# Kernel tuning notes

Hardware: AMD Instinct MI355X
Metric: run time of the kernel (lower is better)

Reference implementation:

```python
import jax, jax.numpy as jnp
import numpy as np

B, N, D = 64, 8192, 128
REPLACE = 0.0  # stands in for torch.inf default; kept finite for numerics


def setup_inputs() -> dict:
    key = jax.random.key(0)
    k1, k2 = jax.random.split(key)
    X = jax.random.normal(k1, (B, N, D), dtype=jnp.float32)
    # mask True == position masked OUT (module computes ~mask to get valid)
    mask = jax.random.randint(k2, (B, N), 0, 2) == 1
    W = jnp.ones((D,), dtype=jnp.float32)
    b = jnp.zeros((D,), dtype=jnp.float32)
    return {"X": X, "mask": mask, "W": W, "b": b}


def reference(X, mask, W, b):
    # valid positions: ~mask, broadcast across feature dim
    valid = (~mask)[:, :, None].astype(X.dtype)          # [B, N, 1]
    count = jnp.sum(valid, axis=1)                       # [B, 1]
    mean = jnp.sum(X * valid, axis=1) / count            # [B, D]
    centered = X - mean[:, None, :]                      # [B, N, D]
    # torch masked std is unbiased (ddof=1)
    var = jnp.sum((centered * centered) * valid, axis=1) / (count - 1.0)
    std = jnp.sqrt(var)                                  # [B, D]
    normed = centered / std[:, None, :]                  # [B, N, D]
    # diag_embed(W) + F.linear == elementwise affine
    out = normed * W + b
    # masked positions were filled with REPLACE before the affine step
    out = jnp.where(mask[:, :, None], REPLACE * W + b, out)
    return out
```

## Files before the change

### kernel.cpp

```cpp
#include <hip/hip_runtime.h>

#define B_ 64
#define N_ 8192
#define D_ 128
#define D4 (D_ / 4)
#define NCHUNKS 16
#define CHUNK (N_ / NCHUNKS)

typedef float v4f __attribute__((ext_vector_type(4)));

#define WS_SUMP  0
#define WS_SQP   (B_ * NCHUNKS * D_)
#define WS_CNTP  (2 * B_ * NCHUNKS * D_)
#define WS_SCALE (2 * B_ * NCHUNKS * D_ + B_ * NCHUNKS)
#define WS_SHIFT (WS_SCALE + B_ * D_)

__global__ __launch_bounds__(256) void reduce_kernel(
        const float* __restrict__ X, const int* __restrict__ mask,
        float* __restrict__ ws) {
    const int b   = blockIdx.x;
    const int cy  = blockIdx.y;
    const int tid = threadIdx.x;
    const int q   = tid & 31;
    const int sub = tid >> 5;
    const int n0  = cy * CHUNK;

    const v4f* __restrict__ Xr = (const v4f*)(X + (size_t)b * N_ * D_);
    const int* __restrict__ mr = mask + b * N_;

    v4f s  = (v4f)(0.f);
    v4f ss = (v4f)(0.f);
    float cnt = 0.f;

    #pragma unroll 4
    for (int k = 0; k < CHUNK / 8; ++k) {
        const int n = n0 + sub + 8 * k;
        const float v = (mr[n] == 0) ? 1.0f : 0.0f;
        v4f x = Xr[(size_t)n * D4 + q];
        x *= v;
        s += x;
        ss += x * x;
        cnt += v;
    }

    __shared__ v4f sh_s[8][32];
    __shared__ v4f sh_ss[8][32];
    __shared__ float sh_c[8];
    sh_s[sub][q]  = s;
    sh_ss[sub][q] = ss;
    if (q == 0) sh_c[sub] = cnt;
    __syncthreads();

    if (sub == 0) {
        v4f ts = s, tss = ss;
        for (int k = 1; k < 8; ++k) {
            ts  += sh_s[k][q];
            tss += sh_ss[k][q];
        }
        v4f* __restrict__ sump = (v4f*)(ws + WS_SUMP);
        v4f* __restrict__ sqp  = (v4f*)(ws + WS_SQP);
        const int slot = (b * NCHUNKS + cy) * D4 + q;
        sump[slot] = ts;
        sqp[slot]  = tss;
    }
    if (tid == 0) {
        float c = 0.f;
        for (int k = 0; k < 8; ++k) c += sh_c[k];
        ws[WS_CNTP + b * NCHUNKS + cy] = c;
    }
}

__global__ __launch_bounds__(256) void finalize_kernel(
        const float* __restrict__ W, const float* __restrict__ bias,
        float* __restrict__ ws) {
    const float* __restrict__ sump = ws + WS_SUMP;
    const float* __restrict__ sqp  = ws + WS_SQP;
    const float* __restrict__ cntp = ws + WS_CNTP;
    float* __restrict__ scale = ws + WS_SCALE;
    float* __restrict__ shift = ws + WS_SHIFT;

    const int i = blockIdx.x * blockDim.x + threadIdx.x;
    if (i >= B_ * D_) return;
    const int b = i >> 7;
    const int d = i & (D_ - 1);

    float c = 0.f, s = 0.f, sq = 0.f;
    #pragma unroll
    for (int cy = 0; cy < NCHUNKS; ++cy) {
        c  += cntp[b * NCHUNKS + cy];
        s  += sump[(b * NCHUNKS + cy) * D_ + d];
        sq += sqp [(b * NCHUNKS + cy) * D_ + d];
    }
    const float mean = s / c;
    const float var  = (sq - s * mean) / (c - 1.0f);
    const float sc   = W[d] * rsqrtf(var);
    scale[i] = sc;
    shift[i] = bias[d] - mean * sc;
}

__global__ __launch_bounds__(256) void normalize_kernel(
        const float* __restrict__ X, const int* __restrict__ mask,
        const float* __restrict__ ws, const float* __restrict__ bias,
        float* __restrict__ out) {
    const v4f* __restrict__ X4 = (const v4f*)X;
    v4f* __restrict__ O4 = (v4f*)out;
    const v4f* __restrict__ S4 = (const v4f*)(ws + WS_SCALE);
    const v4f* __restrict__ H4 = (const v4f*)(ws + WS_SHIFT);
    const v4f* __restrict__ B4 = (const v4f*)bias;

    const long long total = (long long)B_ * N_ * D4;
    long long i = (long long)blockIdx.x * blockDim.x + threadIdx.x;
    const long long stride = (long long)gridDim.x * blockDim.x;

    for (; i < total; i += stride) {
        const int row = (int)(i >> 5);
        const int c   = (int)(i & 31);
        const int b   = row >> 13;
        const int m   = mask[row];
        const v4f x  = X4[i];
        const v4f sc = S4[b * D4 + c];
        const v4f sh = H4[b * D4 + c];
        const v4f bb = B4[c];
        const v4f norm = x * sc + sh;
        v4f o;
        o.x = m ? bb.x : norm.x;
        o.y = m ? bb.y : norm.y;
        o.z = m ? bb.z : norm.z;
        o.w = m ? bb.w : norm.w;
        __builtin_nontemporal_store(o, &O4[i]);
    }
}

extern "C" void kernel_launch(void* const* d_in, const int* in_sizes, int n_in,
                              void* d_out, int out_size, void* d_ws, size_t ws_size,
                              hipStream_t stream) {
    const float* X    = (const float*)d_in[0];
    const int*   mask = (const int*)d_in[1];
    const float* W    = (const float*)d_in[2];
    const float* bias = (const float*)d_in[3];
    float* out = (float*)d_out;
    float* ws  = (float*)d_ws;

    reduce_kernel<<<dim3(B_, NCHUNKS), 256, 0, stream>>>(X, mask, ws);

    finalize_kernel<<<(B_ * D_ + 255) / 256, 256, 0, stream>>>(W, bias, ws);

    normalize_kernel<<<4096, 256, 0, stream>>>(X, mask, ws, bias, out);
}
```

Baseline: 493.3 us.

## Skip loads of masked rows and flatten normalize grid

The reduction kernel now stages the chunk's mask into shared memory, fully unrolls the row loop, and only loads X for valid rows. Chunk count is doubled so more blocks are launched. The normalize kernel drops its grid-stride loop and uses one thread per vec4 with a branch, so masked rows skip reading X and the scale/shift. This aims to cut memory traffic for roughly half the rows, at the cost of divergent control flow and a larger launch grid.

```diff
diff --git a/kernel.cpp b/kernel.cpp
--- a/kernel.cpp
+++ b/kernel.cpp
@@ -4,7 +4,7 @@
 #define N_ 8192
 #define D_ 128
 #define D4 (D_ / 4)
-#define NCHUNKS 16
+#define NCHUNKS 32
 #define CHUNK (N_ / NCHUNKS)
 
 typedef float v4f __attribute__((ext_vector_type(4)));
@@ -25,22 +25,27 @@
     const int sub = tid >> 5;
     const int n0  = cy * CHUNK;
 
-    const v4f* __restrict__ Xr = (const v4f*)(X + (size_t)b * N_ * D_);
-    const int* __restrict__ mr = mask + b * N_;
+    __shared__ float valid[CHUNK];
+    valid[tid] = (mask[b * N_ + n0 + tid] == 0) ? 1.0f : 0.0f;
+    __syncthreads();
+
+    const v4f* __restrict__ Xr =
+        (const v4f*)(X + (size_t)b * N_ * D_) + (size_t)n0 * D4 + q;
 
     v4f s  = (v4f)(0.f);
     v4f ss = (v4f)(0.f);
     float cnt = 0.f;
 
-    #pragma unroll 4
+    #pragma unroll
     for (int k = 0; k < CHUNK / 8; ++k) {
-        const int n = n0 + sub + 8 * k;
-        const float v = (mr[n] == 0) ? 1.0f : 0.0f;
-        v4f x = Xr[(size_t)n * D4 + q];
-        x *= v;
-        s += x;
-        ss += x * x;
+        const int n = sub + 8 * k;
+        const float v = valid[n];
         cnt += v;
+        if (v != 0.0f) {
+            const v4f x = Xr[(size_t)n * D4];
+            s += x;
+            ss += x * x;
+        }
     }
 
     __shared__ v4f sh_s[8][32];
@@ -53,6 +58,7 @@
 
     if (sub == 0) {
         v4f ts = s, tss = ss;
+        #pragma unroll
         for (int k = 1; k < 8; ++k) {
             ts  += sh_s[k][q];
             tss += sh_ss[k][q];
@@ -65,6 +71,7 @@
     }
     if (tid == 0) {
         float c = 0.f;
+        #pragma unroll
         for (int k = 0; k < 8; ++k) c += sh_c[k];
         ws[WS_CNTP + b * NCHUNKS + cy] = c;
     }
@@ -108,26 +115,18 @@
     const v4f* __restrict__ H4 = (const v4f*)(ws + WS_SHIFT);
     const v4f* __restrict__ B4 = (const v4f*)bias;
 
-    const long long total = (long long)B_ * N_ * D4;
-    long long i = (long long)blockIdx.x * blockDim.x + threadIdx.x;
-    const long long stride = (long long)gridDim.x * blockDim.x;
+    const int i   = blockIdx.x * 256 + threadIdx.x;
+    const int row = i >> 5;
+    const int c   = i & 31;
+    const int b   = row >> 13;
 
-    for (; i < total; i += stride) {
-        const int row = (int)(i >> 5);
-        const int c   = (int)(i & 31);
-        const int b   = row >> 13;
-        const int m   = mask[row];
+    if (mask[row] != 0) {
+        __builtin_nontemporal_store(B4[c], &O4[i]);
+    } else {
         const v4f x  = X4[i];
-        const v4f sc = S4[b * D4 + c];
-        const v4f sh = H4[b * D4 + c];
-        const v4f bb = B4[c];
-        const v4f norm = x * sc + sh;
-        v4f o;
-        o.x = m ? bb.x : norm.x;
-        o.y = m ? bb.y : norm.y;
-        o.z = m ? bb.z : norm.z;
-        o.w = m ? bb.w : norm.w;
-        __builtin_nontemporal_store(o, &O4[i]);
+        const v4f sc = S4[(b << 5) + c];
+        const v4f sh = H4[(b << 5) + c];
+        __builtin_nontemporal_store(x * sc + sh, &O4[i]);
     }
 }
 
@@ -145,5 +144,5 @@
 
     finalize_kernel<<<(B_ * D_ + 255) / 256, 256, 0, stream>>>(W, bias, ws);
 
-    normalize_kernel<<<4096, 256, 0, stream>>>(X, mask, ws, bias, out);
+    normalize_kernel<<<(B_ * N_ * D4) / 256, 256, 0, stream>>>(X, mask, ws, bias, out);
 }
```

After: 434.9 us. 1.13x faster.
